# Performance work log

Measured on AMD Instinct MI355X. Metric: run time of the kernel, lower is better.

## Reference

```python
import jax, jax.numpy as jnp
import numpy as np

B, P = 32768, 8
AFF_V, MAT_V, TASK_V, OBJ_V, ST_V = 16, 16, 16, 64, 32
AFF_D = MAT_D = TASK_D = OBJ_D = ST_D = 64
PART_D, OBJ_ENC_D = 256, 256


def setup_inputs() -> dict:
    key = jax.random.key(0)
    ks = jax.random.split(key, 16)
    inp = {
        "aff_idx": jax.random.randint(ks[0], (B, P), 0, AFF_V),
        "mat_idx": jax.random.randint(ks[1], (B, P), 0, MAT_V),
        "task_idx": jax.random.randint(ks[2], (B,), 0, TASK_V),
        "obj_idx": jax.random.randint(ks[3], (B,), 0, OBJ_V),
        "state_idx": jax.random.randint(ks[4], (B,), 0, ST_V),
        "aff_emb": jax.random.normal(ks[5], (AFF_V, AFF_D), jnp.float32),
        "mat_emb": jax.random.normal(ks[6], (MAT_V, MAT_D), jnp.float32),
        "task_emb": jax.random.normal(ks[7], (TASK_V, TASK_D), jnp.float32),
        "obj_emb": jax.random.normal(ks[8], (OBJ_V, OBJ_D), jnp.float32),
        "state_emb": jax.random.normal(ks[9], (ST_V, ST_D), jnp.float32),
        "W_part": jax.random.normal(ks[10], (PART_D, AFF_D + MAT_D), jnp.float32) * 0.05,
        "b_part": jax.random.normal(ks[11], (PART_D,), jnp.float32) * 0.05,
        "W_obj": jax.random.normal(ks[12], (OBJ_ENC_D, TASK_D + OBJ_D + ST_D + PART_D), jnp.float32) * 0.05,
        "b_obj": jax.random.normal(ks[13], (OBJ_ENC_D,), jnp.float32) * 0.05,
    }
    return inp


def reference(aff_idx, mat_idx, task_idx, obj_idx, state_idx,
              aff_emb, mat_emb, task_emb, obj_emb, state_emb,
              W_part, b_part, W_obj, b_obj):
    # Per-part: gather two embeddings, concat, linear, relu  -> [B, P, PART_D]
    part_in = jnp.concatenate([aff_emb[aff_idx], mat_emb[mat_idx]], axis=-1)  # [B,P,128]
    part_enc = jax.nn.relu(jnp.einsum('bpk,ok->bpo', part_in, W_part) + b_part)
    # Max-pool over parts (torch.max values)
    parts_pooled = jnp.max(part_enc, axis=1)  # [B, PART_D]
    # Object-level: concat categorical embeddings with pooled part encoding
    obj_in = jnp.concatenate([task_emb[task_idx], obj_emb[obj_idx],
                              state_emb[state_idx], parts_pooled], axis=-1)  # [B,448]
    return jax.nn.relu(obj_in @ W_obj.T + b_obj)  # [B, OBJ_ENC_D]
```

## Files before the change

kernel.cpp:

```cpp
#include <hip/hip_runtime.h>
#include <hip/hip_bf16.h>


typedef float  f32x4  __attribute__((ext_vector_type(4)));
typedef short  s16x8  __attribute__((ext_vector_type(8)));

__device__ __forceinline__ unsigned short f2bf_rne(float x) {
    unsigned u = __float_as_uint(x);
    u += 0x7FFFu + ((u >> 16) & 1u);
    return (unsigned short)(u >> 16);
}
__device__ __forceinline__ float bf2f(unsigned short s) {
    return __uint_as_float(((unsigned)s) << 16);
}

#define WS_PART_TABLE 0
#define WS_WP2T       131072
#define WS_TT         262144
#define WS_TO         278528
#define WS_TS         344064

__global__ __launch_bounds__(256) void precompute_kernel(
    const float* __restrict__ aff_emb, const float* __restrict__ mat_emb,
    const float* __restrict__ task_emb, const float* __restrict__ obj_emb,
    const float* __restrict__ state_emb,
    const float* __restrict__ W_part, const float* __restrict__ b_part,
    const float* __restrict__ W_obj, const float* __restrict__ b_obj,
    char* __restrict__ ws)
{
    short* part_table = (short*)(ws + WS_PART_TABLE);
    short* wp2t       = (short*)(ws + WS_WP2T);
    float* Tt         = (float*)(ws + WS_TT);
    float* To         = (float*)(ws + WS_TO);
    float* Ts         = (float*)(ws + WS_TS);

    int bid = blockIdx.x, tid = threadIdx.x;
    __shared__ float rowv[128];

    if (bid < 256) {
        int a = bid >> 4, m = bid & 15;
        if (tid < 64)       rowv[tid] = aff_emb[a*64 + tid];
        else if (tid < 128) rowv[tid] = mat_emb[m*64 + (tid-64)];
        __syncthreads();
        float s = b_part[tid];
        const float* w = &W_part[tid*128];
        #pragma unroll
        for (int k = 0; k < 128; k += 4) {
            float4 wv = *(const float4*)&w[k];
            s += rowv[k]*wv.x + rowv[k+1]*wv.y + rowv[k+2]*wv.z + rowv[k+3]*wv.w;
        }
        part_table[bid*256 + tid] = (short)f2bf_rne(fmaxf(s, 0.f));
    } else if (bid < 368) {
        int rr = bid - 256;
        const float* emb; int koff; float* dst;
        if (rr < 16)      { emb = &task_emb[rr*64];        koff = 0;   dst = &Tt[rr*256]; }
        else if (rr < 80) { emb = &obj_emb[(rr-16)*64];    koff = 64;  dst = &To[(rr-16)*256]; }
        else              { emb = &state_emb[(rr-80)*64];  koff = 128; dst = &Ts[(rr-80)*256]; }
        if (tid < 64) rowv[tid] = emb[tid];
        __syncthreads();
        float s = (rr < 16) ? b_obj[tid] : 0.f;
        const float* w = &W_obj[tid*448 + koff];
        #pragma unroll
        for (int k = 0; k < 64; k += 4) {
            float4 wv = *(const float4*)&w[k];
            s += rowv[k]*wv.x + rowv[k+1]*wv.y + rowv[k+2]*wv.z + rowv[k+3]*wv.w;
        }
        dst[tid] = s;
    } else {
        int n = bid - 368;
        wp2t[n*256 + tid] = (short)f2bf_rne(W_obj[n*448 + 192 + tid]);
    }
}

__global__ __launch_bounds__(256, 2) void main_kernel(
    const int* __restrict__ aff_idx, const int* __restrict__ mat_idx,
    const int* __restrict__ task_idx, const int* __restrict__ obj_idx,
    const int* __restrict__ state_idx,
    const char* __restrict__ ws, float* __restrict__ out)
{
    const short* part_table = (const short*)(ws + WS_PART_TABLE);
    const short* wp2t       = (const short*)(ws + WS_WP2T);
    const float* Tt         = (const float*)(ws + WS_TT);
    const float* To         = (const float*)(ws + WS_TO);
    const float* Ts         = (const float*)(ws + WS_TS);

    __shared__ short pooled[16*264];
    __shared__ int   pair_s[16*8];
    __shared__ int   tos_s[48];

    int tid  = threadIdx.x;
    int wave = tid >> 6, lane = tid & 63;
    int l15 = lane & 15, l4 = lane >> 4;

    s16x8 bfrag[4][8];
    #pragma unroll
    for (int nt = 0; nt < 4; ++nt) {
        int n = wave*64 + nt*16 + l15;
        #pragma unroll
        for (int ks = 0; ks < 8; ++ks) {
            int k = ks*32 + l4*8;
            bfrag[nt][ks] = *(const s16x8*)&wp2t[n*256 + k];
        }
    }

    for (int it = 0; it < 4; ++it) {
        int tile = blockIdx.x * 4 + it;
        int row0 = tile * 16;
        __syncthreads();
        if (tid < 128) {
            int r = tid >> 3, j = tid & 7;
            int a = aff_idx[(row0+r)*8 + j];
            int m = mat_idx[(row0+r)*8 + j];
            pair_s[r*8 + j] = (a*16 + m) * 256;
        } else if (tid < 176) {
            int u = tid - 128;
            int r = u & 15, wh = u >> 4;
            int row = row0 + r;
            int v = (wh == 0) ? task_idx[row] : (wh == 1) ? obj_idx[row] : state_idx[row];
            tos_s[wh*16 + r] = v;
        }
        __syncthreads();

        {
            int r = tid >> 4, e = tid & 15;
            float mx[16];
            #pragma unroll
            for (int q = 0; q < 16; ++q) mx[q] = 0.f;
            #pragma unroll
            for (int p = 0; p < 8; ++p) {
                int off = pair_s[r*8 + p] + e*16;
                s16x8 v0 = *(const s16x8*)&part_table[off];
                s16x8 v1 = *(const s16x8*)&part_table[off + 8];
                #pragma unroll
                for (int q = 0; q < 8; ++q) {
                    mx[q]     = fmaxf(mx[q],     bf2f((unsigned short)v0[q]));
                    mx[q + 8] = fmaxf(mx[q + 8], bf2f((unsigned short)v1[q]));
                }
            }
            s16x8 o0, o1;
            #pragma unroll
            for (int q = 0; q < 8; ++q) {
                o0[q] = (short)(__float_as_uint(mx[q])     >> 16);
                o1[q] = (short)(__float_as_uint(mx[q + 8]) >> 16);
            }
            *(s16x8*)&pooled[r*264 + e*16]     = o0;
            *(s16x8*)&pooled[r*264 + e*16 + 8] = o1;
        }
        __syncthreads();

        f32x4 acc[4];
        #pragma unroll
        for (int nt = 0; nt < 4; ++nt) acc[nt] = (f32x4){0.f, 0.f, 0.f, 0.f};
        #pragma unroll
        for (int ks = 0; ks < 8; ++ks) {
            s16x8 af = *(const s16x8*)&pooled[l15*264 + ks*32 + l4*8];
            #pragma unroll
            for (int nt = 0; nt < 4; ++nt)
                acc[nt] = __builtin_amdgcn_mfma_f32_16x16x32_bf16(af, bfrag[nt][ks], acc[nt], 0, 0, 0);
        }

        #pragma unroll
        for (int nt = 0; nt < 4; ++nt) {
            int col = wave*64 + nt*16 + l15;
            #pragma unroll
            for (int reg = 0; reg < 4; ++reg) {
                int rl  = l4*4 + reg;
                int row = row0 + rl;
                int t = tos_s[rl], o = tos_s[16 + rl], s = tos_s[32 + rl];
                float v = acc[nt][reg] + Tt[t*256 + col] + To[o*256 + col] + Ts[s*256 + col];
                out[row*256 + col] = fmaxf(v, 0.f);
            }
        }
    }
}

extern "C" void kernel_launch(void* const* d_in, const int* in_sizes, int n_in,
                              void* d_out, int out_size, void* d_ws, size_t ws_size,
                              hipStream_t stream) {
    const int*   aff_idx   = (const int*)d_in[0];
    const int*   mat_idx   = (const int*)d_in[1];
    const int*   task_idx  = (const int*)d_in[2];
    const int*   obj_idx   = (const int*)d_in[3];
    const int*   state_idx = (const int*)d_in[4];
    const float* aff_emb   = (const float*)d_in[5];
    const float* mat_emb   = (const float*)d_in[6];
    const float* task_emb  = (const float*)d_in[7];
    const float* obj_emb   = (const float*)d_in[8];
    const float* state_emb = (const float*)d_in[9];
    const float* W_part    = (const float*)d_in[10];
    const float* b_part    = (const float*)d_in[11];
    const float* W_obj     = (const float*)d_in[12];
    const float* b_obj     = (const float*)d_in[13];

    precompute_kernel<<<624, 256, 0, stream>>>(
        aff_emb, mat_emb, task_emb, obj_emb, state_emb,
        W_part, b_part, W_obj, b_obj, (char*)d_ws);

    main_kernel<<<512, 256, 0, stream>>>(
        aff_idx, mat_idx, task_idx, obj_idx, state_idx,
        (const char*)d_ws, (float*)d_out);
}
```

Baseline: 117.5 us.

## Process one row tile per block and compare packed bf16 as integers

```diff
diff --git a/kernel.cpp b/kernel.cpp
--- a/kernel.cpp
+++ b/kernel.cpp
@@ -2,16 +2,14 @@
 #include <hip/hip_bf16.h>
 
 
-typedef float  f32x4  __attribute__((ext_vector_type(4)));
-typedef short  s16x8  __attribute__((ext_vector_type(8)));
+typedef float          f32x4  __attribute__((ext_vector_type(4)));
+typedef short          s16x8  __attribute__((ext_vector_type(8)));
+typedef unsigned short u16x8  __attribute__((ext_vector_type(8)));
 
 __device__ __forceinline__ unsigned short f2bf_rne(float x) {
     unsigned u = __float_as_uint(x);
     u += 0x7FFFu + ((u >> 16) & 1u);
     return (unsigned short)(u >> 16);
-}
-__device__ __forceinline__ float bf2f(unsigned short s) {
-    return __uint_as_float(((unsigned)s) << 16);
 }
 
 #define WS_PART_TABLE 0
@@ -72,7 +70,7 @@
     }
 }
 
-__global__ __launch_bounds__(256, 2) void main_kernel(
+__global__ __launch_bounds__(256, 4) void main_kernel(
     const int* __restrict__ aff_idx, const int* __restrict__ mat_idx,
     const int* __restrict__ task_idx, const int* __restrict__ obj_idx,
     const int* __restrict__ state_idx,
@@ -92,84 +90,63 @@
     int wave = tid >> 6, lane = tid & 63;
     int l15 = lane & 15, l4 = lane >> 4;
 
-    s16x8 bfrag[4][8];
+    int row0 = blockIdx.x * 16;
+
+    if (tid < 128) {
+        int r = tid >> 3, j = tid & 7;
+        int a = aff_idx[(row0+r)*8 + j];
+        int m = mat_idx[(row0+r)*8 + j];
+        pair_s[r*8 + j] = (a*16 + m) * 256;
+    } else if (tid < 176) {
+        int u = tid - 128;
+        int r = u & 15, wh = u >> 4;
+        int row = row0 + r;
+        int v = (wh == 0) ? task_idx[row] : (wh == 1) ? obj_idx[row] : state_idx[row];
+        tos_s[wh*16 + r] = v;
+    }
+    __syncthreads();
+
+    {
+        int r = tid >> 4, e = tid & 15;
+        u16x8 mx0 = (u16x8)(0), mx1 = (u16x8)(0);
+        #pragma unroll
+        for (int p = 0; p < 8; ++p) {
+            int off = pair_s[r*8 + p] + e*16;
+            u16x8 v0 = *(const u16x8*)&part_table[off];
+            u16x8 v1 = *(const u16x8*)&part_table[off + 8];
+            mx0 = __builtin_elementwise_max(mx0, v0);
+            mx1 = __builtin_elementwise_max(mx1, v1);
+        }
+        *(u16x8*)&pooled[r*264 + e*16]     = mx0;
+        *(u16x8*)&pooled[r*264 + e*16 + 8] = mx1;
+    }
+    __syncthreads();
+
+    f32x4 acc[4];
     #pragma unroll
-    for (int nt = 0; nt < 4; ++nt) {
-        int n = wave*64 + nt*16 + l15;
+    for (int nt = 0; nt < 4; ++nt) acc[nt] = (f32x4){0.f, 0.f, 0.f, 0.f};
+
+    const short* bbase = &wp2t[(wave*64 + l15)*256 + l4*8];
+    #pragma unroll
+    for (int ks = 0; ks < 8; ++ks) {
+        s16x8 af = *(const s16x8*)&pooled[l15*264 + ks*32 + l4*8];
         #pragma unroll
-        for (int ks = 0; ks < 8; ++ks) {
-            int k = ks*32 + l4*8;
-            bfrag[nt][ks] = *(const s16x8*)&wp2t[n*256 + k];
+        for (int nt = 0; nt < 4; ++nt) {
+            s16x8 bf = *(const s16x8*)&bbase[nt*16*256 + ks*32];
+            acc[nt] = __builtin_amdgcn_mfma_f32_16x16x32_bf16(af, bf, acc[nt], 0, 0, 0);
         }
     }
 
-    for (int it = 0; it < 4; ++it) {
-        int tile = blockIdx.x * 4 + it;
-        int row0 = tile * 16;
-        __syncthreads();
-        if (tid < 128) {
-            int r = tid >> 3, j = tid & 7;
-            int a = aff_idx[(row0+r)*8 + j];
-            int m = mat_idx[(row0+r)*8 + j];
-            pair_s[r*8 + j] = (a*16 + m) * 256;
-        } else if (tid < 176) {
-            int u = tid - 128;
-            int r = u & 15, wh = u >> 4;
-            int row = row0 + r;
-            int v = (wh == 0) ? task_idx[row] : (wh == 1) ? obj_idx[row] : state_idx[row];
-            tos_s[wh*16 + r] = v;
-        }
-        __syncthreads();
-
-        {
-            int r = tid >> 4, e = tid & 15;
-            float mx[16];
-            #pragma unroll
-            for (int q = 0; q < 16; ++q) mx[q] = 0.f;
-            #pragma unroll
-            for (int p = 0; p < 8; ++p) {
-                int off = pair_s[r*8 + p] + e*16;
-                s16x8 v0 = *(const s16x8*)&part_table[off];
-                s16x8 v1 = *(const s16x8*)&part_table[off + 8];
-                #pragma unroll
-                for (int q = 0; q < 8; ++q) {
-                    mx[q]     = fmaxf(mx[q],     bf2f((unsigned short)v0[q]));
-                    mx[q + 8] = fmaxf(mx[q + 8], bf2f((unsigned short)v1[q]));
-                }
-            }
-            s16x8 o0, o1;
-            #pragma unroll
-            for (int q = 0; q < 8; ++q) {
-                o0[q] = (short)(__float_as_uint(mx[q])     >> 16);
-                o1[q] = (short)(__float_as_uint(mx[q + 8]) >> 16);
-            }
-            *(s16x8*)&pooled[r*264 + e*16]     = o0;
-            *(s16x8*)&pooled[r*264 + e*16 + 8] = o1;
-        }
-        __syncthreads();
-
-        f32x4 acc[4];
+    #pragma unroll
+    for (int nt = 0; nt < 4; ++nt) {
+        int col = wave*64 + nt*16 + l15;
         #pragma unroll
-        for (int nt = 0; nt < 4; ++nt) acc[nt] = (f32x4){0.f, 0.f, 0.f, 0.f};
-        #pragma unroll
-        for (int ks = 0; ks < 8; ++ks) {
-            s16x8 af = *(const s16x8*)&pooled[l15*264 + ks*32 + l4*8];
-            #pragma unroll
-            for (int nt = 0; nt < 4; ++nt)
-                acc[nt] = __builtin_amdgcn_mfma_f32_16x16x32_bf16(af, bfrag[nt][ks], acc[nt], 0, 0, 0);
-        }
-
-        #pragma unroll
-        for (int nt = 0; nt < 4; ++nt) {
-            int col = wave*64 + nt*16 + l15;
-            #pragma unroll
-            for (int reg = 0; reg < 4; ++reg) {
-                int rl  = l4*4 + reg;
-                int row = row0 + rl;
-                int t = tos_s[rl], o = tos_s[16 + rl], s = tos_s[32 + rl];
-                float v = acc[nt][reg] + Tt[t*256 + col] + To[o*256 + col] + Ts[s*256 + col];
-                out[row*256 + col] = fmaxf(v, 0.f);
-            }
+        for (int reg = 0; reg < 4; ++reg) {
+            int rl  = l4*4 + reg;
+            int row = row0 + rl;
+            int t = tos_s[rl], o = tos_s[16 + rl], s = tos_s[32 + rl];
+            float v = acc[nt][reg] + Tt[t*256 + col] + To[o*256 + col] + Ts[s*256 + col];
+            out[row*256 + col] = fmaxf(v, 0.f);
         }
     }
 }
@@ -196,7 +173,7 @@
         aff_emb, mat_emb, task_emb, obj_emb, state_emb,
         W_part, b_part, W_obj, b_obj, (char*)d_ws);
 
-    main_kernel<<<512, 256, 0, stream>>>(
+    main_kernel<<<2048, 256, 0, stream>>>(
         aff_idx, mat_idx, task_idx, obj_idx, state_idx,
         (const char*)d_ws, (float*)d_out);
 }
```

Measured after the change: 135.5 us. 1.15x slower.
